# Kernel optimization log

Hardware: AMD Instinct MI355X
Metric: run time of the kernel (lower is better)

Reference implementation:

```python
import jax, jax.numpy as jnp
import numpy as np

B, T, S, D = 4, 2048, 4, 1024
SINKHORN_ITERS = 20
EPS = 1e-8


def sinkhorn(matrix, iterations=SINKHORN_ITERS, eps=EPS):
    # Project onto doubly stochastic matrices via alternating normalization.
    P = jnp.exp(matrix - jnp.max(matrix, axis=-1, keepdims=True))
    def body(_, P):
        P = P / (jnp.sum(P, axis=-1, keepdims=True) + eps)
        P = P / (jnp.sum(P, axis=-2, keepdims=True) + eps)
        return P
    return jax.lax.fori_loop(0, iterations, body, P)


def setup_inputs() -> dict:
    key = jax.random.key(0)
    k1, k2, k3 = jax.random.split(key, 3)
    x = jax.random.normal(k1, (B, T, S, D), dtype=jnp.float32)
    layer_output = jax.random.normal(k2, (B, T, D), dtype=jnp.float32)
    H_res = jax.random.normal(k3, (S, S), dtype=jnp.float32) * 0.01
    H_pos = jnp.full((S, 1), 1.0 / S, dtype=jnp.float32)
    alpha_res = jnp.float32(0.01)
    alpha_pos = jnp.float32(0.01)
    bias_res = jnp.zeros((S, D), dtype=jnp.float32)
    bias_pos = jnp.zeros((S, D), dtype=jnp.float32)
    return {"x": x, "layer_output": layer_output, "H_res": H_res,
            "H_pos": H_pos, "alpha_res": alpha_res, "alpha_pos": alpha_pos,
            "bias_res": bias_res, "bias_pos": bias_pos}


def reference(x, layer_output, H_res, H_pos, alpha_res, alpha_pos, bias_res, bias_pos):
    H_res_proj = sinkhorn(H_res)  # (S, S) doubly stochastic
    # mix streams: [B,T,S,D] x [S,R] -> [B,T,R,D]
    x_mixed = jnp.einsum('btsd,sr->btrd', x, H_res_proj)
    x_mixed = alpha_res * x_mixed + bias_res[None, None, :, :]
    # broadcast layer output across streams, scaled per-stream by H_pos
    layer_out = layer_output[:, :, None, :] * H_pos[None, None, :, :]  # (B,T,S,D)
    layer_out = alpha_pos * layer_out + bias_pos[None, None, :, :]
    return x + x_mixed + layer_out
```

## Files before the change

### kernel.cpp

```cpp
#include <hip/hip_runtime.h>
#include <hip/hip_bf16.h>

constexpr int Bc = 4;
constexpr int Tc = 2048;
constexpr int Sc = 4;
constexpr int Dc = 1024;
constexpr int BT = Bc * Tc;
constexpr int SD = Sc * Dc;
constexpr int SINKHORN_ITERS = 20;
constexpr int NBLK = 2048;

typedef float vfloat4 __attribute__((ext_vector_type(4)));

__global__ __launch_bounds__(256) void fused_kernel(
        const float* __restrict__ x,
        const float* __restrict__ lo,
        const float* __restrict__ Hres,
        const float* __restrict__ Hpos,
        const float* __restrict__ alpha_res,
        const float* __restrict__ alpha_pos,
        const float* __restrict__ bias_res,
        const float* __restrict__ bias_pos,
        float* __restrict__ out) {
    __shared__ float s_aH[16];
    __shared__ float s_hp[4];

    const int tid = threadIdx.x;
    if (tid < 16) {
        const int i = tid >> 2;
        const int j = tid & 3;
        const float h = Hres[i * 4 + j];
        float m = fmaxf(h, __shfl_xor(h, 1));
        m = fmaxf(m, __shfl_xor(m, 2));
        float P = __expf(h - m);
        for (int it = 0; it < SINKHORN_ITERS; ++it) {
            float s = P + __shfl_xor(P, 1);
            s += __shfl_xor(s, 2);
            P *= __builtin_amdgcn_rcpf(s + 1e-8f);
            float c = P + __shfl_xor(P, 4);
            c += __shfl_xor(c, 8);
            P *= __builtin_amdgcn_rcpf(c + 1e-8f);
        }
        s_aH[j * 4 + i] = alpha_res[0] * P;
        if (i == 0) s_hp[j] = alpha_pos[0] * Hpos[j];
    }
    __syncthreads();

    float aH[4][4];
#pragma unroll
    for (int r = 0; r < 4; ++r)
#pragma unroll
        for (int s = 0; s < 4; ++s) aH[r][s] = s_aH[r * 4 + s];
    const float hpr[4] = {s_hp[0], s_hp[1], s_hp[2], s_hp[3]};

    const int d0 = tid << 2;
    float cb[4][4];
#pragma unroll
    for (int r = 0; r < 4; ++r) {
        const vfloat4 br = *reinterpret_cast<const vfloat4*>(bias_res + r * Dc + d0);
        const vfloat4 bp = *reinterpret_cast<const vfloat4*>(bias_pos + r * Dc + d0);
        cb[r][0] = br.x + bp.x; cb[r][1] = br.y + bp.y;
        cb[r][2] = br.z + bp.z; cb[r][3] = br.w + bp.w;
    }

#pragma unroll
    for (int it = 0; it < BT / NBLK; ++it) {
        const int bt = blockIdx.x + it * NBLK;
        const int xbase = bt * SD + d0;

        float xs[4][4];
#pragma unroll
        for (int s = 0; s < 4; ++s) {
            const vfloat4 v = *reinterpret_cast<const vfloat4*>(x + xbase + s * Dc);
            xs[s][0] = v.x; xs[s][1] = v.y; xs[s][2] = v.z; xs[s][3] = v.w;
        }
        const vfloat4 lv = *reinterpret_cast<const vfloat4*>(lo + bt * Dc + d0);
        const float lf[4] = {lv.x, lv.y, lv.z, lv.w};

#pragma unroll
        for (int r = 0; r < 4; ++r) {
            float acc[4];
#pragma unroll
            for (int j = 0; j < 4; ++j)
                acc[j] = fmaf(lf[j], hpr[r], xs[r][j] + cb[r][j]);
#pragma unroll
            for (int s = 0; s < 4; ++s)
#pragma unroll
                for (int j = 0; j < 4; ++j)
                    acc[j] = fmaf(xs[s][j], aH[r][s], acc[j]);
            vfloat4 o;
            o.x = acc[0]; o.y = acc[1]; o.z = acc[2]; o.w = acc[3];
            __builtin_nontemporal_store(o, reinterpret_cast<vfloat4*>(out + xbase + r * Dc));
        }
    }
}

extern "C" void kernel_launch(void* const* d_in, const int* in_sizes, int n_in,
                              void* d_out, int out_size, void* d_ws, size_t ws_size,
                              hipStream_t stream) {
    const float* x         = (const float*)d_in[0];
    const float* layer_out = (const float*)d_in[1];
    const float* H_res     = (const float*)d_in[2];
    const float* H_pos     = (const float*)d_in[3];
    const float* alpha_res = (const float*)d_in[4];
    const float* alpha_pos = (const float*)d_in[5];
    const float* bias_res  = (const float*)d_in[6];
    const float* bias_pos  = (const float*)d_in[7];
    float* out = (float*)d_out;

    fused_kernel<<<NBLK, 256, 0, stream>>>(x, layer_out, H_res, H_pos,
                                           alpha_res, alpha_pos,
                                           bias_res, bias_pos, out);
}
```

Baseline: 267.3 us.

## Prefetch first tile before Sinkhorn and double-buffer row loads

Issues the first tile's global loads before the Sinkhorn prologue and barrier, so their memory latency overlaps the small projection computation. The per-row loop becomes a manual two-buffer software pipeline that loads the next tile before computing and storing the current one. Combined biases now live in shared memory instead of registers, and the uniform coefficients are forced into scalar registers with readfirstlane. This raises register pressure from keeping two tiles in flight and adds LDS reads per row.

```diff
diff --git a/kernel.cpp b/kernel.cpp
--- a/kernel.cpp
+++ b/kernel.cpp
@@ -1,5 +1,4 @@
 #include <hip/hip_runtime.h>
-#include <hip/hip_bf16.h>
 
 constexpr int Bc = 4;
 constexpr int Tc = 2048;
@@ -11,6 +10,10 @@
 constexpr int NBLK = 2048;
 
 typedef float vfloat4 __attribute__((ext_vector_type(4)));
+
+__device__ __forceinline__ float uniform_f(float v) {
+    return __uint_as_float(__builtin_amdgcn_readfirstlane(__float_as_uint(v)));
+}
 
 __global__ __launch_bounds__(256) void fused_kernel(
         const float* __restrict__ x,
@@ -24,8 +27,26 @@
         float* __restrict__ out) {
     __shared__ float s_aH[16];
     __shared__ float s_hp[4];
+    __shared__ vfloat4 s_cb[4 * 256];
 
     const int tid = threadIdx.x;
+    const int d0 = tid << 2;
+    const int bt0 = blockIdx.x;
+
+    const float* xp0 = x + bt0 * SD + d0;
+    vfloat4 a0 = *reinterpret_cast<const vfloat4*>(xp0);
+    vfloat4 a1 = *reinterpret_cast<const vfloat4*>(xp0 + Dc);
+    vfloat4 a2 = *reinterpret_cast<const vfloat4*>(xp0 + 2 * Dc);
+    vfloat4 a3 = *reinterpret_cast<const vfloat4*>(xp0 + 3 * Dc);
+    vfloat4 al = *reinterpret_cast<const vfloat4*>(lo + bt0 * Dc + d0);
+
+#pragma unroll
+    for (int r = 0; r < 4; ++r) {
+        const vfloat4 br = *reinterpret_cast<const vfloat4*>(bias_res + r * Dc + d0);
+        const vfloat4 bp = *reinterpret_cast<const vfloat4*>(bias_pos + r * Dc + d0);
+        s_cb[r * 256 + tid] = br + bp;
+    }
+
     if (tid < 16) {
         const int i = tid >> 2;
         const int j = tid & 3;
@@ -47,52 +68,52 @@
     __syncthreads();
 
     float aH[4][4];
-#pragma unroll
-    for (int r = 0; r < 4; ++r)
-#pragma unroll
-        for (int s = 0; s < 4; ++s) aH[r][s] = s_aH[r * 4 + s];
-    const float hpr[4] = {s_hp[0], s_hp[1], s_hp[2], s_hp[3]};
-
-    const int d0 = tid << 2;
-    float cb[4][4];
+    float hp[4];
 #pragma unroll
     for (int r = 0; r < 4; ++r) {
-        const vfloat4 br = *reinterpret_cast<const vfloat4*>(bias_res + r * Dc + d0);
-        const vfloat4 bp = *reinterpret_cast<const vfloat4*>(bias_pos + r * Dc + d0);
-        cb[r][0] = br.x + bp.x; cb[r][1] = br.y + bp.y;
-        cb[r][2] = br.z + bp.z; cb[r][3] = br.w + bp.w;
+#pragma unroll
+        for (int s = 0; s < 4; ++s) aH[r][s] = uniform_f(s_aH[r * 4 + s]);
+        hp[r] = uniform_f(s_hp[r]);
     }
 
-#pragma unroll
-    for (int it = 0; it < BT / NBLK; ++it) {
-        const int bt = blockIdx.x + it * NBLK;
-        const int xbase = bt * SD + d0;
+    auto load_tile = [&](int bt, vfloat4& x0, vfloat4& x1, vfloat4& x2,
+                         vfloat4& x3, vfloat4& lv) {
+        const float* xp = x + bt * SD + d0;
+        x0 = *reinterpret_cast<const vfloat4*>(xp);
+        x1 = *reinterpret_cast<const vfloat4*>(xp + Dc);
+        x2 = *reinterpret_cast<const vfloat4*>(xp + 2 * Dc);
+        x3 = *reinterpret_cast<const vfloat4*>(xp + 3 * Dc);
+        lv = *reinterpret_cast<const vfloat4*>(lo + bt * Dc + d0);
+    };
 
-        float xs[4][4];
-#pragma unroll
-        for (int s = 0; s < 4; ++s) {
-            const vfloat4 v = *reinterpret_cast<const vfloat4*>(x + xbase + s * Dc);
-            xs[s][0] = v.x; xs[s][1] = v.y; xs[s][2] = v.z; xs[s][3] = v.w;
-        }
-        const vfloat4 lv = *reinterpret_cast<const vfloat4*>(lo + bt * Dc + d0);
-        const float lf[4] = {lv.x, lv.y, lv.z, lv.w};
-
+    auto compute_store = [&](int bt, vfloat4 x0, vfloat4 x1, vfloat4 x2,
+                             vfloat4 x3, vfloat4 lv) {
+        float* op = out + bt * SD + d0;
+        vfloat4 xs[4] = {x0, x1, x2, x3};
 #pragma unroll
         for (int r = 0; r < 4; ++r) {
-            float acc[4];
+            const vfloat4 cb = s_cb[r * 256 + tid];
+            vfloat4 acc;
 #pragma unroll
             for (int j = 0; j < 4; ++j)
-                acc[j] = fmaf(lf[j], hpr[r], xs[r][j] + cb[r][j]);
+                acc[j] = fmaf(lv[j], hp[r], xs[r][j] + cb[j]);
 #pragma unroll
             for (int s = 0; s < 4; ++s)
 #pragma unroll
                 for (int j = 0; j < 4; ++j)
                     acc[j] = fmaf(xs[s][j], aH[r][s], acc[j]);
-            vfloat4 o;
-            o.x = acc[0]; o.y = acc[1]; o.z = acc[2]; o.w = acc[3];
-            __builtin_nontemporal_store(o, reinterpret_cast<vfloat4*>(out + xbase + r * Dc));
+            __builtin_nontemporal_store(acc, reinterpret_cast<vfloat4*>(op + r * Dc));
         }
-    }
+    };
+
+    vfloat4 b0, b1, b2, b3, bl;
+    load_tile(bt0 + NBLK, b0, b1, b2, b3, bl);
+    compute_store(bt0, a0, a1, a2, a3, al);
+    load_tile(bt0 + 2 * NBLK, a0, a1, a2, a3, al);
+    compute_store(bt0 + NBLK, b0, b1, b2, b3, bl);
+    load_tile(bt0 + 3 * NBLK, b0, b1, b2, b3, bl);
+    compute_store(bt0 + 2 * NBLK, a0, a1, a2, a3, al);
+    compute_store(bt0 + 3 * NBLK, b0, b1, b2, b3, bl);
 }
 
 extern "C" void kernel_launch(void* const* d_in, const int* in_sizes, int n_in,
```

New measurement: 265.0 us. No clear change (-0.8%).

## Compute Sinkhorn per wavefront with readlane broadcast, one block per row

Applied to the files above, without the earlier changes.

The kernel no longer has a single group of 16 threads compute the Sinkhorn projection and share it through LDS behind a __syncthreads. Every wavefront now computes it redundantly in registers and broadcasts the coefficients with readlane. The x, layer-output and bias loads are issued before the Sinkhorn loop so their memory latency overlaps the serial shuffle chain. The grid grows to one block per (b,t) row with an occupancy hint, and the nontemporal stores become plain stores, which may change cache behaviour on a streaming write.

```diff
diff --git a/kernel.cpp b/kernel.cpp
--- a/kernel.cpp
+++ b/kernel.cpp
@@ -1,18 +1,17 @@
 #include <hip/hip_runtime.h>
-#include <hip/hip_bf16.h>
 
-constexpr int Bc = 4;
-constexpr int Tc = 2048;
-constexpr int Sc = 4;
 constexpr int Dc = 1024;
-constexpr int BT = Bc * Tc;
-constexpr int SD = Sc * Dc;
+constexpr int SD = 4 * Dc;
 constexpr int SINKHORN_ITERS = 20;
-constexpr int NBLK = 2048;
+constexpr int NBLK = 8192;
 
 typedef float vfloat4 __attribute__((ext_vector_type(4)));
 
-__global__ __launch_bounds__(256) void fused_kernel(
+__device__ __forceinline__ float readlane_f(float v, int lane) {
+    return __uint_as_float(__builtin_amdgcn_readlane(__float_as_uint(v), lane));
+}
+
+__global__ __launch_bounds__(256, 8) void fused_kernel(
         const float* __restrict__ x,
         const float* __restrict__ lo,
         const float* __restrict__ Hres,
@@ -22,76 +21,69 @@
         const float* __restrict__ bias_res,
         const float* __restrict__ bias_pos,
         float* __restrict__ out) {
-    __shared__ float s_aH[16];
-    __shared__ float s_hp[4];
+    const int tid  = threadIdx.x;
+    const int lane = tid & 63;
+    const int d0   = tid << 2;
+    const int bt   = blockIdx.x;
 
-    const int tid = threadIdx.x;
-    if (tid < 16) {
-        const int i = tid >> 2;
-        const int j = tid & 3;
-        const float h = Hres[i * 4 + j];
-        float m = fmaxf(h, __shfl_xor(h, 1));
-        m = fmaxf(m, __shfl_xor(m, 2));
-        float P = __expf(h - m);
-        for (int it = 0; it < SINKHORN_ITERS; ++it) {
-            float s = P + __shfl_xor(P, 1);
-            s += __shfl_xor(s, 2);
-            P *= __builtin_amdgcn_rcpf(s + 1e-8f);
-            float c = P + __shfl_xor(P, 4);
-            c += __shfl_xor(c, 8);
-            P *= __builtin_amdgcn_rcpf(c + 1e-8f);
-        }
-        s_aH[j * 4 + i] = alpha_res[0] * P;
-        if (i == 0) s_hp[j] = alpha_pos[0] * Hpos[j];
-    }
-    __syncthreads();
+    const float* xp = x + bt * SD + d0;
+    const vfloat4 x0 = *reinterpret_cast<const vfloat4*>(xp);
+    const vfloat4 x1 = *reinterpret_cast<const vfloat4*>(xp + Dc);
+    const vfloat4 x2 = *reinterpret_cast<const vfloat4*>(xp + 2 * Dc);
+    const vfloat4 x3 = *reinterpret_cast<const vfloat4*>(xp + 3 * Dc);
+    const vfloat4 lv = *reinterpret_cast<const vfloat4*>(lo + bt * Dc + d0);
 
-    float aH[4][4];
-#pragma unroll
-    for (int r = 0; r < 4; ++r)
-#pragma unroll
-        for (int s = 0; s < 4; ++s) aH[r][s] = s_aH[r * 4 + s];
-    const float hpr[4] = {s_hp[0], s_hp[1], s_hp[2], s_hp[3]};
-
-    const int d0 = tid << 2;
-    float cb[4][4];
+    vfloat4 cb[4];
 #pragma unroll
     for (int r = 0; r < 4; ++r) {
         const vfloat4 br = *reinterpret_cast<const vfloat4*>(bias_res + r * Dc + d0);
         const vfloat4 bp = *reinterpret_cast<const vfloat4*>(bias_pos + r * Dc + d0);
-        cb[r][0] = br.x + bp.x; cb[r][1] = br.y + bp.y;
-        cb[r][2] = br.z + bp.z; cb[r][3] = br.w + bp.w;
+        cb[r] = br + bp;
     }
 
+    const int i = (lane >> 2) & 3;
+    const int j = lane & 3;
+    const float h   = Hres[i * 4 + j];
+    const float hpv = Hpos[j];
+    const float a_res = alpha_res[0];
+    const float a_pos = alpha_pos[0];
+
+    float m = fmaxf(h, __shfl_xor(h, 1));
+    m = fmaxf(m, __shfl_xor(m, 2));
+    float P = __expf(h - m);
 #pragma unroll
-    for (int it = 0; it < BT / NBLK; ++it) {
-        const int bt = blockIdx.x + it * NBLK;
-        const int xbase = bt * SD + d0;
+    for (int it = 0; it < SINKHORN_ITERS; ++it) {
+        float s = P + __shfl_xor(P, 1);
+        s += __shfl_xor(s, 2);
+        P *= __builtin_amdgcn_rcpf(s + 1e-8f);
+        float c = P + __shfl_xor(P, 4);
+        c += __shfl_xor(c, 8);
+        P *= __builtin_amdgcn_rcpf(c + 1e-8f);
+    }
 
-        float xs[4][4];
+    const float aP = a_res * P;
+    float aH[4][4], hp[4];
 #pragma unroll
-        for (int s = 0; s < 4; ++s) {
-            const vfloat4 v = *reinterpret_cast<const vfloat4*>(x + xbase + s * Dc);
-            xs[s][0] = v.x; xs[s][1] = v.y; xs[s][2] = v.z; xs[s][3] = v.w;
-        }
-        const vfloat4 lv = *reinterpret_cast<const vfloat4*>(lo + bt * Dc + d0);
-        const float lf[4] = {lv.x, lv.y, lv.z, lv.w};
+    for (int r = 0; r < 4; ++r) {
+#pragma unroll
+        for (int s = 0; s < 4; ++s) aH[r][s] = readlane_f(aP, 4 * s + r);
+        hp[r] = a_pos * readlane_f(hpv, r);
+    }
 
+    const vfloat4 xs[4] = {x0, x1, x2, x3};
+    float* op = out + bt * SD + d0;
 #pragma unroll
-        for (int r = 0; r < 4; ++r) {
-            float acc[4];
+    for (int r = 0; r < 4; ++r) {
+        vfloat4 acc;
 #pragma unroll
-            for (int j = 0; j < 4; ++j)
-                acc[j] = fmaf(lf[j], hpr[r], xs[r][j] + cb[r][j]);
+        for (int jj = 0; jj < 4; ++jj)
+            acc[jj] = fmaf(lv[jj], hp[r], xs[r][jj] + cb[r][jj]);
 #pragma unroll
-            for (int s = 0; s < 4; ++s)
+        for (int s = 0; s < 4; ++s)
 #pragma unroll
-                for (int j = 0; j < 4; ++j)
-                    acc[j] = fmaf(xs[s][j], aH[r][s], acc[j]);
-            vfloat4 o;
-            o.x = acc[0]; o.y = acc[1]; o.z = acc[2]; o.w = acc[3];
-            __builtin_nontemporal_store(o, reinterpret_cast<vfloat4*>(out + xbase + r * Dc));
-        }
+            for (int jj = 0; jj < 4; ++jj)
+                acc[jj] = fmaf(xs[s][jj], aH[r][s], acc[jj]);
+        *reinterpret_cast<vfloat4*>(op + r * Dc) = acc;
     }
 }
 
```

Result: no change. 264.2 us (-1.2%).
